# Kernel tuning notes

Measured on AMD Instinct MI355X. Metric: run time of the kernel, lower is better.

The kernel has to match this reference:

```python
import jax, jax.numpy as jnp
import numpy as np

S = 64        # state_dim
M = 16        # message_dim
H = 128       # hidden_unit_message_dim
HR = 128      # hidden_unit_readout_dim
NSTEPS = 10
N_NODES = 10000
N_FACTORS = 40000


def setup_inputs() -> dict:
    rng = np.random.default_rng(0)
    n, F = N_NODES, N_FACTORS
    # random undirected factor pairs (u, v) with u < v
    u = rng.integers(0, n - 1, F)
    v = rng.integers(u + 1, n)
    # var->factor directed edges: (u, i) and (v, i) for factor i
    v2f_src = np.stack([u, v], 1).ravel().astype(np.int32)          # [E]
    v2f_dst = np.repeat(np.arange(F), 2).astype(np.int32)           # [E]
    b = rng.normal(size=n).astype(np.float32)
    Juv = rng.normal(size=F).astype(np.float32)
    Jvu = rng.normal(size=F).astype(np.float32)
    feat_u = np.stack([b[u], b[v], Juv, Jvu], 1)
    feat_v = np.stack([b[v], b[u], Juv, Jvu], 1)
    feat = np.stack([feat_u, feat_v], 1).reshape(-1, 4).astype(np.float32)  # [E,4]
    p = lambda *s: (0.1 * rng.normal(size=s)).astype(np.float32)
    z = lambda *s: np.zeros(s, np.float32)
    inp = {
        'v2f_src': jnp.asarray(v2f_src), 'v2f_dst': jnp.asarray(v2f_dst),
        'f2v_src': jnp.asarray(v2f_dst), 'f2v_dst': jnp.asarray(v2f_src),
        'feat_v2f': jnp.asarray(feat), 'feat_f2v': jnp.asarray(feat),
        'n_nodes': n, 'n_factors': F,
        'Qw': jnp.asarray(p(4, M * M)), 'Qb': jnp.asarray(z(M * M)),
        'mp1_w1': jnp.asarray(p(2 * S, H)), 'mp1_b1': jnp.asarray(z(H)),
        'mp1_w2': jnp.asarray(p(H, H)), 'mp1_b2': jnp.asarray(z(H)),
        'mp1_w3': jnp.asarray(p(H, M)), 'mp1_b3': jnp.asarray(z(M)),
        'mp2_w1': jnp.asarray(p(2 * S, H)), 'mp2_b1': jnp.asarray(z(H)),
        'mp2_w2': jnp.asarray(p(H, H)), 'mp2_b2': jnp.asarray(z(H)),
        'mp2_w3': jnp.asarray(p(H, M)), 'mp2_b3': jnp.asarray(z(M)),
        'g1_wih': jnp.asarray(p(M, 3 * S)), 'g1_whh': jnp.asarray(p(S, 3 * S)),
        'g1_bih': jnp.asarray(z(3 * S)), 'g1_bhh': jnp.asarray(z(3 * S)),
        'g2_wih': jnp.asarray(p(M, 3 * S)), 'g2_whh': jnp.asarray(p(S, 3 * S)),
        'g2_bih': jnp.asarray(z(3 * S)), 'g2_bhh': jnp.asarray(z(3 * S)),
        'ro_w1': jnp.asarray(p(S, HR)), 'ro_b1': jnp.asarray(z(HR)),
        'ro_w2': jnp.asarray(p(HR, HR)), 'ro_b2': jnp.asarray(z(HR)),
        'ro_w3': jnp.asarray(p(HR, 2)), 'ro_b3': jnp.asarray(z(2)),
    }
    return inp


def _mlp(x, w1, b1, w2, b2, w3, b3):
    h = jax.nn.relu(x @ w1 + b1)
    h = jax.nn.relu(h @ w2 + b2)
    return h @ w3 + b3


def _gru(x, h, wih, whh, bih, bhh):
    # torch.nn.GRUCell gate order: r, z, n
    gi = x @ wih + bih
    gh = h @ whh + bhh
    ir, iz, inn = jnp.split(gi, 3, axis=-1)
    hr, hz, hn = jnp.split(gh, 3, axis=-1)
    r = jax.nn.sigmoid(ir + hr)
    zg = jax.nn.sigmoid(iz + hz)
    ng = jnp.tanh(inn + r * hn)
    return (1.0 - zg) * ng + zg * h


def reference(v2f_src, v2f_dst, f2v_src, f2v_dst, feat_v2f, feat_f2v,
              n_nodes, n_factors, Qw, Qb,
              mp1_w1, mp1_b1, mp1_w2, mp1_b2, mp1_w3, mp1_b3,
              mp2_w1, mp2_b1, mp2_w2, mp2_b2, mp2_w3, mp2_b3,
              g1_wih, g1_whh, g1_bih, g1_bhh,
              g2_wih, g2_whh, g2_bih, g2_bhh,
              ro_w1, ro_b1, ro_w2, ro_b2, ro_w3, ro_b3):
    var_h = jnp.zeros((n_nodes, S), feat_v2f.dtype)
    fac_h = jnp.zeros((n_factors, S), feat_v2f.dtype)
    # per-edge transform matrices are the same every step; hoist out of the loop
    q1 = (feat_v2f @ Qw + Qb).reshape(-1, M, M)  # [E, M, M]
    q2 = (feat_f2v @ Qw + Qb).reshape(-1, M, M)
    for _ in range(NSTEPS):
        # var -> factor
        x = jnp.concatenate([var_h[v2f_src], fac_h[v2f_dst]], axis=-1)  # [E, 2S]
        m = _mlp(x, mp1_w1, mp1_b1, mp1_w2, mp1_b2, mp1_w3, mp1_b3)    # [E, M]
        m = jnp.einsum('eij,ej->ei', q1, m)
        fac_msg = jax.ops.segment_sum(m, v2f_dst, num_segments=n_factors)
        fac_h = _gru(fac_msg, fac_h, g1_wih, g1_whh, g1_bih, g1_bhh)
        # factor -> var
        x = jnp.concatenate([fac_h[f2v_src], var_h[f2v_dst]], axis=-1)
        m = _mlp(x, mp2_w1, mp2_b1, mp2_w2, mp2_b2, mp2_w3, mp2_b3)
        m = jnp.einsum('eij,ej->ei', q2, m)
        var_msg = jax.ops.segment_sum(m, f2v_dst, num_segments=n_nodes)
        var_h = _gru(var_msg, var_h, g2_wih, g2_whh, g2_bih, g2_bhh)
    out = _mlp(var_h, ro_w1, ro_b1, ro_w2, ro_b2, ro_w3, ro_b3)  # [n_nodes, 2]
    return jax.nn.softmax(out, axis=1)
```

## Files before the change

kernel.cpp:

```cpp
#include <hip/hip_runtime.h>

#define NSTEPS 10

typedef __attribute__((ext_vector_type(8))) short bf16x8;
typedef __attribute__((ext_vector_type(4))) float f32x4;

__device__ __forceinline__ float sigmoidf_(float x) { return 1.0f / (1.0f + __expf(-x)); }
__device__ __forceinline__ float tanh_fast(float x) {
  const float e = __expf(2.f * x);
  return 1.f - 2.f / (e + 1.f);
}
__device__ __forceinline__ short bf16_(float x) {
  union { float f; unsigned u; } c; c.f = x;
  unsigned r = (c.u + 0x7FFFu + ((c.u >> 16) & 1u)) >> 16;
  return (short)r;
}
__device__ __forceinline__ unsigned pk2_(float a, float b) {
  union { float f; unsigned u; } ca, cb; ca.f = a; cb.f = b;
  return __builtin_amdgcn_perm(cb.u + 0x8000u, ca.u + 0x8000u, 0x07060302u);
}
__device__ __forceinline__ short pk1_(float a) {
  union { float f; unsigned u; } c; c.f = a;
  return (short)((c.u + 0x8000u) >> 16);
}
__device__ __forceinline__ float lo_(unsigned u) { union { unsigned u; float f; } c; c.u = u << 16; return c.f; }
__device__ __forceinline__ float hi_(unsigned u) { union { unsigned u; float f; } c; c.u = u & 0xffff0000u; return c.f; }

__device__ __forceinline__ f32x4 mfma_16x16x32(bf16x8 a, bf16x8 b, f32x4 c) {
  return __builtin_amdgcn_mfma_f32_16x16x32_bf16(a, b, c, 0, 0, 0);
}

#define C_W2A   0
#define C_W2B   32
#define C_W3A   64
#define C_W3B   68
#define C_ACOMB 72
#define C_W1AD  104
#define C_W1BS  120
#define C_RO1   136
#define C_RO2   152
#define C_Q     184
#define C_G1    189
#define C_G2    237
#define TOTAL_CHUNKS 285

struct PackJob { const float* src; int N; int KS; int nchunks; };
struct PackArgs {
  PackJob jb[10];
  const float* Qw; const float* Qb;
  const float* g1wih; const float* g1whh;
  const float* g2wih; const float* g2whh;
};

__device__ __forceinline__ float pack_val(const PackArgs& a, int g) {
  int c = g >> 9;
  const int r = g & 511;
  const int j = r & 7, n = (r >> 3) & 15, q = (r >> 7) & 3;
  const int kq = q * 8 + j;
  float val = 0.f;
  bool done = false;
  #pragma unroll
  for (int ji = 0; ji < 10; ++ji) {
    if (!done && c < a.jb[ji].nchunks) {
      const int ks = c % a.jb[ji].KS;
      const int nt = c / a.jb[ji].KS;
      const int k = ks * 32 + kq;
      val = a.jb[ji].src[(size_t)k * a.jb[ji].N + nt * 16 + n];
      done = true;
    }
    if (!done) c -= a.jb[ji].nchunks;
  }
  if (!done) {
    if (c < 5) {
      val = 0.f;
      if (kq < 16) val = (c < 4) ? a.Qw[c * 256 + n * 16 + kq] : a.Qb[n * 16 + kq];
    } else {
      c -= 5;
      const float* wih = (c < 48) ? a.g1wih : a.g2wih;
      const float* whh = (c < 48) ? a.g1whh : a.g2whh;
      if (c >= 48) c -= 48;
      const int nt = c / 3, ks = c % 3;
      const int k = ks * 32 + kq;
      const int ng = nt * 16 + n;
      const int gate = ng >> 6, s = ng & 63;
      val = 0.f;
      if (gate == 0) {
        if (k < 16) val = wih[k * 192 + s];
        else if (k < 80) val = whh[(k - 16) * 192 + s];
      } else if (gate == 1) {
        if (k < 16) val = wih[k * 192 + 64 + s];
        else if (k < 80) val = whh[(k - 16) * 192 + 64 + s];
      } else if (gate == 2) {
        if (k < 16) val = wih[k * 192 + 128 + s];
      } else {
        if (k >= 16 && k < 80) val = whh[(k - 16) * 192 + 128 + s];
      }
    }
  }
  return val;
}

__global__ __launch_bounds__(256) void k_pack(PackArgs a, short* __restrict__ out, int total) {
  const int g = blockIdx.x * 256 + threadIdx.x;
  if (g < total) out[g] = bf16_(pack_val(a, g));
}

__device__ __forceinline__ void edge_tail(
    const short* wb, int cw2, int cw3,
    const float* b2, const float* b3,
    short* h1s, short* ms, const float* feats,
    int lane, int wave, int m, int quad, float* mq)
{
  f32x4 acc2[2][4] = {};
  #pragma unroll
  for (int ks = 0; ks < 4; ++ks) {
    bf16x8 afr[4];
    #pragma unroll
    for (int mt = 0; mt < 4; ++mt)
      afr[mt] = *(const bf16x8*)&h1s[(mt * 16 + m) * 136 + ks * 32 + quad * 8];
    #pragma unroll
    for (int nt2 = 0; nt2 < 2; ++nt2) {
      const bf16x8 bfr = ((const bf16x8*)(wb + cw2))[((wave * 2 + nt2) * 4 + ks) * 64 + lane];
      #pragma unroll
      for (int mt = 0; mt < 4; ++mt)
        acc2[nt2][mt] = mfma_16x16x32(afr[mt], bfr, acc2[nt2][mt]);
    }
  }
  __syncthreads();
  #pragma unroll
  for (int nt2 = 0; nt2 < 2; ++nt2) {
    const int col = (wave * 2 + nt2) * 16 + m;
    const float bv = b2[col];
    #pragma unroll
    for (int mt = 0; mt < 4; ++mt)
      #pragma unroll
      for (int rr = 0; rr < 4; ++rr)
        h1s[(mt * 16 + quad * 4 + rr) * 136 + col] =
            pk1_(fmaxf(acc2[nt2][mt][rr] + bv, 0.f));
  }
  __syncthreads();
  f32x4 acc3 = {};
  #pragma unroll
  for (int ks = 0; ks < 4; ++ks) {
    const bf16x8 afr = *(const bf16x8*)&h1s[(wave * 16 + m) * 136 + ks * 32 + quad * 8];
    acc3 = mfma_16x16x32(afr, ((const bf16x8*)(wb + cw3))[ks * 64 + lane], acc3);
  }
  const float b3v = b3[m];
  #pragma unroll
  for (int rr = 0; rr < 4; ++rr) {
    const int row = wave * 16 + quad * 4 + rr;
    ms[row * 40 + m] = pk1_(acc3[rr] + b3v);
    ms[row * 40 + 16 + m] = 0;
  }
  __syncthreads();
  f32x4 accY[5] = {};
  {
    const bf16x8 afr = *(const bf16x8*)&ms[(wave * 16 + m) * 40 + quad * 8];
    #pragma unroll
    for (int tq = 0; tq < 5; ++tq)
      accY[tq] = mfma_16x16x32(afr, ((const bf16x8*)(wb + C_Q * 512))[tq * 64 + lane], accY[tq]);
  }
  #pragma unroll
  for (int rr = 0; rr < 4; ++rr) {
    const int row = wave * 16 + quad * 4 + rr;
    const f32x4 f = *(const f32x4*)&feats[row * 4];
    mq[rr] = accY[4][rr] + f.x * accY[0][rr] + f.y * accY[1][rr]
                         + f.z * accY[2][rr] + f.w * accY[3][rr];
  }
}

__device__ __forceinline__ void var_gru_tile(
    const short* wb, const float* gbih, const float* gbhh,
    const short* SA, float* gruH, short* outTile, int outStr,
    int rbase, int Nn, int lane, int wave, int m, int quad, bool writeH)
{
  f32x4 acc[16] = {};
  #pragma unroll
  for (int ks = 0; ks < 3; ++ks) {
    const bf16x8 av = *(const bf16x8*)&SA[(wave * 16 + m) * 104 + ks * 32 + quad * 8];
    #pragma unroll
    for (int nt = 0; nt < 16; ++nt)
      acc[nt] = mfma_16x16x32(av, ((const bf16x8*)(wb + C_G2 * 512))[(nt * 3 + ks) * 64 + lane], acc[nt]);
  }
  #pragma unroll
  for (int nt = 0; nt < 4; ++nt) {
    const int s = nt * 16 + m;
    const float br  = gbih[s] + gbhh[s];
    const float bz  = gbih[64 + s] + gbhh[64 + s];
    const float bin = gbih[128 + s];
    const float bhn = gbhh[128 + s];
    #pragma unroll
    for (int reg = 0; reg < 4; ++reg) {
      const int lr = wave * 16 + quad * 4 + reg, rg = rbase + lr;
      short hv = 0;
      if (rg < Nn) {
        const float ho = gruH[(size_t)rg * 64 + s];
        const float rr = sigmoidf_(acc[nt][reg] + br);
        const float zz = sigmoidf_(acc[4 + nt][reg] + bz);
        const float nn = tanh_fast(acc[8 + nt][reg] + bin + rr * (acc[12 + nt][reg] + bhn));
        const float hn = (1.f - zz) * nn + zz * ho;
        if (writeH) gruH[(size_t)rg * 64 + s] = hn;
        hv = pk1_(hn);
      }
      outTile[lr * outStr + s] = hv;
    }
  }
}

__global__ __launch_bounds__(256) void k_phaseA(
    const float* __restrict__ msgIn, float* __restrict__ msgZero,
    float* __restrict__ var_h,
    short* __restrict__ Abuf, short* __restrict__ Bbuf,
    const short* __restrict__ wb,
    const float* __restrict__ gbih, const float* __restrict__ gbhh, int N)
{
  __shared__ short SA[64 * 104];
  __shared__ short Xs[64 * 72];
  const int t = threadIdx.x, lane = t & 63, wave = t >> 6;
  const int m = lane & 15, quad = lane >> 4;
  const int rbase = blockIdx.x * 64;

  if (msgIn) {
    {
      const int r = t >> 2, q4 = t & 3, rg = rbase + r;
      #pragma unroll
      for (int i = 0; i < 6; ++i) {
        const int c = q4 * 4 + i * 16;
        f32x4 v = {0.f, 0.f, 0.f, 0.f};
        if (rg < N) {
          if (c < 16)      v = *(const f32x4*)(msgIn + (size_t)rg * 16 + c);
          else if (c < 80) v = *(const f32x4*)(var_h + (size_t)rg * 64 + (c - 16));
        }
        *(unsigned*)&SA[r * 104 + c]     = pk2_(v.x, v.y);
        *(unsigned*)&SA[r * 104 + c + 2] = pk2_(v.z, v.w);
      }
      if (rbase + r < N) {
        f32x4 z = {0.f, 0.f, 0.f, 0.f};
        *(f32x4*)(msgZero + (size_t)(rbase + r) * 16 + q4 * 4) = z;
      }
    }
    __syncthreads();
    var_gru_tile(wb, gbih, gbhh, SA, var_h, Xs, 72,
                 rbase, N, lane, wave, m, quad, true);
    __syncthreads();
  } else {
    const int r = t >> 2, q4 = t & 3, rg = rbase + r;
    #pragma unroll
    for (int i = 0; i < 4; ++i) {
      const int cc = q4 * 4 + i * 16;
      f32x4 v = {0.f, 0.f, 0.f, 0.f};
      if (rg < N) v = *(const f32x4*)(var_h + (size_t)rg * 64 + cc);
      *(unsigned*)&Xs[r * 72 + cc]     = pk2_(v.x, v.y);
      *(unsigned*)&Xs[r * 72 + cc + 2] = pk2_(v.z, v.w);
    }
    __syncthreads();
  }

  f32x4 acc[4][4] = {};
  #pragma unroll
  for (int ks = 0; ks < 2; ++ks) {
    bf16x8 afr[4];
    #pragma unroll
    for (int mt = 0; mt < 4; ++mt)
      afr[mt] = *(const bf16x8*)&Xs[(mt * 16 + m) * 72 + ks * 32 + quad * 8];
    #pragma unroll
    for (int j = 0; j < 4; ++j) {
      const bf16x8 bfr = ((const bf16x8*)(wb + C_ACOMB * 512))[((wave * 4 + j) * 2 + ks) * 64 + lane];
      #pragma unroll
      for (int mt = 0; mt < 4; ++mt)
        acc[j][mt] = mfma_16x16x32(afr[mt], bfr, acc[j][mt]);
    }
  }
  #pragma unroll
  for (int j = 0; j < 4; ++j) {
    const int col = (wave * 4 + j) * 16 + m;
    short* dst = (col < 128) ? Abuf : Bbuf;
    const int c2 = col & 127;
    #pragma unroll
    for (int mt = 0; mt < 4; ++mt)
      #pragma unroll
      for (int reg = 0; reg < 4; ++reg) {
        const int rg = rbase + mt * 16 + quad * 4 + reg;
        if (rg < N) dst[(size_t)rg * 128 + c2] = pk1_(acc[j][mt][reg]);
      }
  }
}

__global__ __launch_bounds__(256) void k_phaseB(
    const short* __restrict__ Abuf, const short* __restrict__ Bbuf,
    const int* __restrict__ v2f_src, const int* __restrict__ f2v_dst,
    const float* __restrict__ featA, const float* __restrict__ featB,
    const float* __restrict__ m1b1, const float* __restrict__ m1b2,
    const float* __restrict__ m1b3,
    const float* __restrict__ m2b1, const float* __restrict__ m2b2,
    const float* __restrict__ m2b3,
    const float* __restrict__ g1bih, const float* __restrict__ g1bhh,
    const short* __restrict__ wb,
    float* __restrict__ fac_h, float* __restrict__ msgV, int E, int F)
{
  __shared__ short AsG[32 * 104];
  __shared__ short Ps[32 * 136];
  __shared__ short h1s[64 * 136];
  __shared__ short ms[64 * 40];
  __shared__ short Fs2[32 * 72];
  __shared__ float feats[64 * 4];
  __shared__ int sidx[64], didx[64];

  const int t = threadIdx.x, lane = t & 63, wave = t >> 6;
  const int m = lane & 15, quad = lane >> 4;
  const int e0 = blockIdx.x * 64, f0 = blockIdx.x * 32;

  if (t < 64) {
    const int eg = e0 + t;
    sidx[t] = (eg < E) ? v2f_src[eg] : 0;
    didx[t] = (eg < E) ? f2v_dst[eg] : 0;
  }
  {
    const int e = t >> 2, k = t & 3, eg = e0 + e;
    feats[e * 4 + k] = (eg < E) ? featA[(size_t)eg * 4 + k] : 0.f;
  }
  {
    const int hr = t >> 3, hc = (t & 7) * 8;
    const int f = f0 + hr;
    f32x4 a0 = {0.f,0.f,0.f,0.f}, a1 = {0.f,0.f,0.f,0.f};
    if (f < F) {
      a0 = *(const f32x4*)(fac_h + (size_t)f * 64 + hc);
      a1 = *(const f32x4*)(fac_h + (size_t)f * 64 + hc + 4);
    }
    uint4 o;
    o.x = pk2_(a0.x, a0.y); o.y = pk2_(a0.z, a0.w);
    o.z = pk2_(a1.x, a1.y); o.w = pk2_(a1.z, a1.w);
    *(uint4*)&AsG[hr * 104 + 16 + hc] = o;
    if (t < 64) {
      uint4 z = make_uint4(0u, 0u, 0u, 0u);
      *(uint4*)&AsG[(t >> 1) * 104 + 80 + (t & 1) * 8] = z;
    }
  }
  __syncthreads();

  {
    const int mt = wave & 1, ng = wave >> 1;
    f32x4 pacc[4] = {};
    #pragma unroll
    for (int ks = 0; ks < 2; ++ks) {
      const bf16x8 av = *(const bf16x8*)&AsG[(mt * 16 + m) * 104 + 16 + ks * 32 + quad * 8];
      #pragma unroll
      for (int j = 0; j < 4; ++j) {
        const bf16x8 bfr = ((const bf16x8*)(wb + C_W1AD * 512))[((ng * 4 + j) * 2 + ks) * 64 + lane];
        pacc[j] = mfma_16x16x32(av, bfr, pacc[j]);
      }
    }
    #pragma unroll
    for (int j = 0; j < 4; ++j) {
      const int col = (ng * 4 + j) * 16 + m;
      #pragma unroll
      for (int reg = 0; reg < 4; ++reg)
        Ps[(mt * 16 + quad * 4 + reg) * 136 + col] = pk1_(pacc[j][reg]);
    }
  }
  __syncthreads();

  {
    const int r = t >> 2, q4 = t & 3;
    const bool ok = (e0 + r) < E;
    const short* pa = Abuf + (size_t)sidx[r] * 128;
    const short* pb = Ps + (r >> 1) * 136;
    #pragma unroll
    for (int i = 0; i < 4; ++i) {
      const int col = (q4 + i * 4) * 8;
      uint4 o = make_uint4(0u, 0u, 0u, 0u);
      if (ok) {
        const uint4 ua = *(const uint4*)(pa + col);
        const uint4 ub = *(const uint4*)(pb + col);
        const f32x4 ba = *(const f32x4*)(m1b1 + col);
        const f32x4 bb = *(const f32x4*)(m1b1 + col + 4);
        o.x = pk2_(fmaxf(lo_(ua.x) + lo_(ub.x) + ba.x, 0.f),
                   fmaxf(hi_(ua.x) + hi_(ub.x) + ba.y, 0.f));
        o.y = pk2_(fmaxf(lo_(ua.y) + lo_(ub.y) + ba.z, 0.f),
                   fmaxf(hi_(ua.y) + hi_(ub.y) + ba.w, 0.f));
        o.z = pk2_(fmaxf(lo_(ua.z) + lo_(ub.z) + bb.x, 0.f),
                   fmaxf(hi_(ua.z) + hi_(ub.z) + bb.y, 0.f));
        o.w = pk2_(fmaxf(lo_(ua.w) + lo_(ub.w) + bb.z, 0.f),
                   fmaxf(hi_(ua.w) + hi_(ub.w) + bb.w, 0.f));
      }
      *(uint4*)&h1s[r * 136 + col] = o;
    }
  }
  __syncthreads();

  float mq[4];
  edge_tail(wb, C_W2A * 512, C_W3A * 512, m1b2, m1b3,
            h1s, ms, feats, lane, wave, m, quad, mq);
  {
    const int fl = wave * 8 + quad * 2;
    AsG[fl * 104 + m]       = pk1_(mq[0] + mq[1]);
    AsG[(fl + 1) * 104 + m] = pk1_(mq[2] + mq[3]);
  }
  __syncthreads();

  {
    const int mtg = wave >> 1, sh = wave & 1;
    f32x4 accG[8] = {};
    #pragma unroll
    for (int ks = 0; ks < 3; ++ks) {
      const bf16x8 av = *(const bf16x8*)&AsG[(mtg * 16 + m) * 104 + ks * 32 + quad * 8];
      #pragma unroll
      for (int g = 0; g < 4; ++g)
        #pragma unroll
        for (int nt2 = 0; nt2 < 2; ++nt2) {
          const int nt = g * 4 + sh * 2 + nt2;
          accG[g * 2 + nt2] = mfma_16x16x32(
              av, ((const bf16x8*)(wb + C_G1 * 512))[(nt * 3 + ks) * 64 + lane],
              accG[g * 2 + nt2]);
        }
    }
    #pragma unroll
    for (int nt2 = 0; nt2 < 2; ++nt2) {
      const int s = sh * 32 + nt2 * 16 + m;
      const float br  = g1bih[s] + g1bhh[s];
      const float bz  = g1bih[64 + s] + g1bhh[64 + s];
      const float bin = g1bih[128 + s];
      const float bhn = g1bhh[128 + s];
      #pragma unroll
      for (int reg = 0; reg < 4; ++reg) {
        const int lr = mtg * 16 + quad * 4 + reg;
        const int f = f0 + lr;
        short hv = 0;
        if (f < F) {
          const float ho = fac_h[(size_t)f * 64 + s];
          const float rr = sigmoidf_(accG[nt2][reg] + br);
          const float zz = sigmoidf_(accG[2 + nt2][reg] + bz);
          const float nn = tanh_fast(accG[4 + nt2][reg] + bin +
                                     rr * (accG[6 + nt2][reg] + bhn));
          const float hn = (1.f - zz) * nn + zz * ho;
          fac_h[(size_t)f * 64 + s] = hn;
          hv = pk1_(hn);
        }
        Fs2[lr * 72 + s] = hv;
      }
    }
  }
  {
    const int e = t >> 2, k = t & 3, eg = e0 + e;
    feats[e * 4 + k] = (eg < E) ? featB[(size_t)eg * 4 + k] : 0.f;
  }
  __syncthreads();

  {
    const int mt = wave & 1, ng = wave >> 1;
    f32x4 pacc[4] = {};
    #pragma unroll
    for (int ks = 0; ks < 2; ++ks) {
      const bf16x8 av = *(const bf16x8*)&Fs2[(mt * 16 + m) * 72 + ks * 32 + quad * 8];
      #pragma unroll
      for (int j = 0; j < 4; ++j) {
        const bf16x8 bfr = ((const bf16x8*)(wb + C_W1BS * 512))[((ng * 4 + j) * 2 + ks) * 64 + lane];
        pacc[j] = mfma_16x16x32(av, bfr, pacc[j]);
      }
    }
    #pragma unroll
    for (int j = 0; j < 4; ++j) {
      const int col = (ng * 4 + j) * 16 + m;
      #pragma unroll
      for (int reg = 0; reg < 4; ++reg)
        Ps[(mt * 16 + quad * 4 + reg) * 136 + col] = pk1_(pacc[j][reg]);
    }
  }
  __syncthreads();

  {
    const int r = t >> 2, q4 = t & 3;
    const bool ok = (e0 + r) < E;
    const short* pa = Ps + (r >> 1) * 136;
    const short* pb = Bbuf + (size_t)didx[r] * 128;
    #pragma unroll
    for (int i = 0; i < 4; ++i) {
      const int col = (q4 + i * 4) * 8;
      uint4 o = make_uint4(0u, 0u, 0u, 0u);
      if (ok) {
        const uint4 ua = *(const uint4*)(pa + col);
        const uint4 ub = *(const uint4*)(pb + col);
        const f32x4 ba = *(const f32x4*)(m2b1 + col);
        const f32x4 bb = *(const f32x4*)(m2b1 + col + 4);
        o.x = pk2_(fmaxf(lo_(ua.x) + lo_(ub.x) + ba.x, 0.f),
                   fmaxf(hi_(ua.x) + hi_(ub.x) + ba.y, 0.f));
        o.y = pk2_(fmaxf(lo_(ua.y) + lo_(ub.y) + ba.z, 0.f),
                   fmaxf(hi_(ua.y) + hi_(ub.y) + ba.w, 0.f));
        o.z = pk2_(fmaxf(lo_(ua.z) + lo_(ub.z) + bb.x, 0.f),
                   fmaxf(hi_(ua.z) + hi_(ub.z) + bb.y, 0.f));
        o.w = pk2_(fmaxf(lo_(ua.w) + lo_(ub.w) + bb.z, 0.f),
                   fmaxf(hi_(ua.w) + hi_(ub.w) + bb.w, 0.f));
      }
      *(uint4*)&h1s[r * 136 + col] = o;
    }
  }
  __syncthreads();

  float mq2[4];
  edge_tail(wb, C_W2B * 512, C_W3B * 512, m2b2, m2b3,
            h1s, ms, feats, lane, wave, m, quad, mq2);
  #pragma unroll
  for (int rr = 0; rr < 4; ++rr) {
    const int erow = wave * 16 + quad * 4 + rr;
    if (e0 + erow < E)
      atomicAdd(msgV + (size_t)didx[erow] * 16 + m, mq2[rr]);
  }
}

__global__ __launch_bounds__(256) void k_readout_f(
    const float* __restrict__ gruMsg, const float* __restrict__ gruH,
    const short* __restrict__ wb,
    const float* __restrict__ gbih, const float* __restrict__ gbhh,
    const float* __restrict__ rob1, const float* __restrict__ rob2,
    const float* __restrict__ row3, const float* __restrict__ rob3,
    float* __restrict__ out, int rows)
{
  __shared__ short SA[64 * 104];
  __shared__ short SH[64 * 72];
  __shared__ short S1[64 * 136];
  __shared__ short S2[64 * 136];
  __shared__ float w3s[256];
  const int t = threadIdx.x, lane = t & 63, wave = t >> 6;
  const int m = lane & 15, quad = lane >> 4;
  const int rbase = blockIdx.x * 64;

  w3s[t] = row3[t];
  {
    const int r = t >> 2, q4 = t & 3, rg = rbase + r;
    #pragma unroll
    for (int i = 0; i < 6; ++i) {
      const int c = q4 * 4 + i * 16;
      f32x4 v = {0.f, 0.f, 0.f, 0.f};
      if (rg < rows) {
        if (c < 16)      v = *(const f32x4*)(gruMsg + (size_t)rg * 16 + c);
        else if (c < 80) v = *(const f32x4*)(gruH + (size_t)rg * 64 + (c - 16));
      }
      *(unsigned*)&SA[r * 104 + c]     = pk2_(v.x, v.y);
      *(unsigned*)&SA[r * 104 + c + 2] = pk2_(v.z, v.w);
    }
  }
  __syncthreads();
  var_gru_tile(wb, gbih, gbhh, SA, (float*)gruH, SH, 72,
               rbase, rows, lane, wave, m, quad, false);
  __syncthreads();
  {
    f32x4 acc[2][4] = {};
    #pragma unroll
    for (int ks = 0; ks < 2; ++ks) {
      bf16x8 afr[4];
      #pragma unroll
      for (int mt = 0; mt < 4; ++mt)
        afr[mt] = *(const bf16x8*)&SH[(mt * 16 + m) * 72 + ks * 32 + quad * 8];
      #pragma unroll
      for (int nt2 = 0; nt2 < 2; ++nt2) {
        const bf16x8 bfr = ((const bf16x8*)(wb + C_RO1 * 512))[((wave * 2 + nt2) * 2 + ks) * 64 + lane];
        #pragma unroll
        for (int mt = 0; mt < 4; ++mt)
          acc[nt2][mt] = mfma_16x16x32(afr[mt], bfr, acc[nt2][mt]);
      }
    }
    #pragma unroll
    for (int nt2 = 0; nt2 < 2; ++nt2) {
      const int col = (wave * 2 + nt2) * 16 + m;
      const float bv = rob1[col];
      #pragma unroll
      for (int mt = 0; mt < 4; ++mt)
        #pragma unroll
        for (int rr = 0; rr < 4; ++rr)
          S1[(mt * 16 + quad * 4 + rr) * 136 + col] =
              pk1_(fmaxf(acc[nt2][mt][rr] + bv, 0.f));
    }
  }
  __syncthreads();
  {
    f32x4 acc[2][4] = {};
    #pragma unroll
    for (int ks = 0; ks < 4; ++ks) {
      bf16x8 afr[4];
      #pragma unroll
      for (int mt = 0; mt < 4; ++mt)
        afr[mt] = *(const bf16x8*)&S1[(mt * 16 + m) * 136 + ks * 32 + quad * 8];
      #pragma unroll
      for (int nt2 = 0; nt2 < 2; ++nt2) {
        const bf16x8 bfr = ((const bf16x8*)(wb + C_RO2 * 512))[((wave * 2 + nt2) * 4 + ks) * 64 + lane];
        #pragma unroll
        for (int mt = 0; mt < 4; ++mt)
          acc[nt2][mt] = mfma_16x16x32(afr[mt], bfr, acc[nt2][mt]);
      }
    }
    #pragma unroll
    for (int nt2 = 0; nt2 < 2; ++nt2) {
      const int col = (wave * 2 + nt2) * 16 + m;
      const float bv = rob2[col];
      #pragma unroll
      for (int mt = 0; mt < 4; ++mt)
        #pragma unroll
        for (int rr = 0; rr < 4; ++rr)
          S2[(mt * 16 + quad * 4 + rr) * 136 + col] =
              pk1_(fmaxf(acc[nt2][mt][rr] + bv, 0.f));
    }
  }
  __syncthreads();
  if (t < 64) {
    const int rg = rbase + t;
    if (rg < rows) {
      float l0 = rob3[0], l1 = rob3[1];
      #pragma unroll 8
      for (int k = 0; k < 128; k += 2) {
        const unsigned u = *(const unsigned*)&S2[t * 136 + k];
        const float x0 = lo_(u), x1 = hi_(u);
        l0 = fmaf(x0, w3s[k * 2 + 0], l0);
        l1 = fmaf(x0, w3s[k * 2 + 1], l1);
        l0 = fmaf(x1, w3s[k * 2 + 2], l0);
        l1 = fmaf(x1, w3s[k * 2 + 3], l1);
      }
      const float mx = fmaxf(l0, l1);
      const float e0 = __expf(l0 - mx), e1 = __expf(l1 - mx);
      const float inv = 1.f / (e0 + e1);
      out[(size_t)rg * 2 + 0] = e0 * inv;
      out[(size_t)rg * 2 + 1] = e1 * inv;
    }
  }
}

extern "C" void kernel_launch(void* const* d_in, const int* in_sizes, int n_in,
                              void* d_out, int out_size, void* d_ws, size_t ws_size,
                              hipStream_t stream)
{
  const int*   v2f_src  = (const int*)d_in[0];
  const int*   f2v_dst  = (const int*)d_in[3];
  const float* feat_v2f = (const float*)d_in[4];
  const float* feat_f2v = (const float*)d_in[5];
  const float* Qw    = (const float*)d_in[8];
  const float* Qb    = (const float*)d_in[9];
  const float* m1w1  = (const float*)d_in[10];
  const float* m1b1  = (const float*)d_in[11];
  const float* m1w2  = (const float*)d_in[12];
  const float* m1b2  = (const float*)d_in[13];
  const float* m1w3  = (const float*)d_in[14];
  const float* m1b3  = (const float*)d_in[15];
  const float* m2w1  = (const float*)d_in[16];
  const float* m2b1  = (const float*)d_in[17];
  const float* m2w2  = (const float*)d_in[18];
  const float* m2b2  = (const float*)d_in[19];
  const float* m2w3  = (const float*)d_in[20];
  const float* m2b3  = (const float*)d_in[21];
  const float* g1wih = (const float*)d_in[22];
  const float* g1whh = (const float*)d_in[23];
  const float* g1bih = (const float*)d_in[24];
  const float* g1bhh = (const float*)d_in[25];
  const float* g2wih = (const float*)d_in[26];
  const float* g2whh = (const float*)d_in[27];
  const float* g2bih = (const float*)d_in[28];
  const float* g2bhh = (const float*)d_in[29];
  const float* row1  = (const float*)d_in[30];
  const float* rob1  = (const float*)d_in[31];
  const float* row2  = (const float*)d_in[32];
  const float* rob2  = (const float*)d_in[33];
  const float* row3  = (const float*)d_in[34];
  const float* rob3  = (const float*)d_in[35];

  const int E = in_sizes[0];
  const int N = out_size / 2;
  const int F = E / 2;

  float* wsf   = (float*)d_ws;
  float* var_h = wsf;
  float* fac_h = var_h + (size_t)N * 64;
  float* msgV  = fac_h + (size_t)F * 64;
  short* Abuf  = (short*)(msgV + (size_t)N * 16);
  short* Bbuf  = Abuf + (size_t)N * 128;
  short* wb    = Bbuf + (size_t)N * 128;

  hipMemsetAsync(var_h, 0,
                 ((size_t)N * 64 + (size_t)F * 64 + (size_t)N * 16) * sizeof(float),
                 stream);

  PackArgs pk;
  pk.jb[0] = {m1w2,            128, 4, 32};
  pk.jb[1] = {m2w2,            128, 4, 32};
  pk.jb[2] = {m1w3,             16, 4,  4};
  pk.jb[3] = {m2w3,             16, 4,  4};
  pk.jb[4] = {m1w1,            128, 2, 16};
  pk.jb[5] = {m2w1 + 64 * 128, 128, 2, 16};
  pk.jb[6] = {m1w1 + 64 * 128, 128, 2, 16};
  pk.jb[7] = {m2w1,            128, 2, 16};
  pk.jb[8] = {row1,            128, 2, 16};
  pk.jb[9] = {row2,            128, 4, 32};
  pk.Qw = Qw; pk.Qb = Qb;
  pk.g1wih = g1wih; pk.g1whh = g1whh;
  pk.g2wih = g2wih; pk.g2whh = g2whh;
  const int packTotal = TOTAL_CHUNKS * 512;
  k_pack<<<(packTotal + 255) / 256, 256, 0, stream>>>(pk, wb, packTotal);

  const int gN = (N + 63) / 64;
  const int gE = (E + 63) / 64;

  for (int step = 0; step < NSTEPS; ++step) {
    k_phaseA<<<gN, 256, 0, stream>>>(
        step ? msgV : nullptr, msgV, var_h, Abuf, Bbuf, wb, g2bih, g2bhh, N);
    k_phaseB<<<gE, 256, 0, stream>>>(
        Abuf, Bbuf, v2f_src, f2v_dst, feat_v2f, feat_f2v,
        m1b1, m1b2, m1b3, m2b1, m2b2, m2b3, g1bih, g1bhh,
        wb, fac_h, msgV, E, F);
  }

  k_readout_f<<<gN, 256, 0, stream>>>(
      msgV, var_h, wb, g2bih, g2bhh, rob1, rob2, row3, rob3, (float*)d_out, N);
}
```

Measured before the change: 706.1 us.

## Transpose MFMA operand roles so outputs store as packed row vectors

Several small GEMMs (MLP layer 2, readout layers, A/B combine, partial W1 products) now put the weight fragment in the A operand and the activation tile in the B operand. Each lane then holds four consecutive output columns of one row, so results are written as packed uint2 bf16 stores instead of scattered 16-bit stores. The GRU weight packing permutes the state index to match, which makes the GRU epilogue vectorised too (f32x4/float2 loads and stores of hidden state, packed tile writes). In edge_tail this also drops one barrier, and shared memory is merged into one aliased buffer to cut LDS use, which relies on the aliased regions never being live at the same time.

```diff
diff --git a/kernel.cpp b/kernel.cpp
--- a/kernel.cpp
+++ b/kernel.cpp
@@ -82,7 +82,9 @@
       const int nt = c / 3, ks = c % 3;
       const int k = ks * 32 + kq;
       const int ng = nt * 16 + n;
-      const int gate = ng >> 6, s = ng & 63;
+      const int gate = ng >> 6;
+      const int nq = ng & 63;
+      const int s = (nq & 15) * 4 + (nq >> 4);
       val = 0.f;
       if (gate == 0) {
         if (k < 16) val = wih[k * 192 + s];
@@ -105,40 +107,98 @@
   if (g < total) out[g] = bf16_(pack_val(a, g));
 }
 
+__device__ __forceinline__ void var_gru_tile(
+    const short* wb, const float* gbih, const float* gbhh,
+    const short* SA, float* gruH, short* outTile, int outStr,
+    int rbase, int Nn, int lane, int wave, int m, int quad, bool writeH)
+{
+  f32x4 acc[16] = {};
+  #pragma unroll
+  for (int ks = 0; ks < 3; ++ks) {
+    const bf16x8 av = *(const bf16x8*)&SA[(wave * 16 + m) * 104 + ks * 32 + quad * 8];
+    #pragma unroll
+    for (int nt = 0; nt < 16; ++nt)
+      acc[nt] = mfma_16x16x32(av, ((const bf16x8*)(wb + C_G2 * 512))[(nt * 3 + ks) * 64 + lane], acc[nt]);
+  }
+  const int sb = m * 4;
+  const f32x4 bir = *(const f32x4*)(gbih + sb);
+  const f32x4 bhr = *(const f32x4*)(gbhh + sb);
+  const f32x4 biz = *(const f32x4*)(gbih + 64 + sb);
+  const f32x4 bhz = *(const f32x4*)(gbhh + 64 + sb);
+  const f32x4 bi4 = *(const f32x4*)(gbih + 128 + sb);
+  const f32x4 bh4 = *(const f32x4*)(gbhh + 128 + sb);
+  #pragma unroll
+  for (int reg = 0; reg < 4; ++reg) {
+    const int lr = wave * 16 + quad * 4 + reg, rg = rbase + lr;
+    uint2 pv; pv.x = 0u; pv.y = 0u;
+    if (rg < Nn) {
+      const f32x4 ho = *(const f32x4*)(gruH + (size_t)rg * 64 + sb);
+      f32x4 hn;
+      #pragma unroll
+      for (int nt = 0; nt < 4; ++nt) {
+        const float rr = sigmoidf_(acc[nt][reg] + bir[nt] + bhr[nt]);
+        const float zz = sigmoidf_(acc[4 + nt][reg] + biz[nt] + bhz[nt]);
+        const float nn = tanh_fast(acc[8 + nt][reg] + bi4[nt] + rr * (acc[12 + nt][reg] + bh4[nt]));
+        hn[nt] = (1.f - zz) * nn + zz * ho[nt];
+      }
+      if (writeH) *(f32x4*)(gruH + (size_t)rg * 64 + sb) = hn;
+      pv.x = pk2_(hn[0], hn[1]);
+      pv.y = pk2_(hn[2], hn[3]);
+    }
+    *(uint2*)&outTile[lr * outStr + sb] = pv;
+  }
+}
+
+__device__ __forceinline__ void partial_gemm_T(
+    const short* chunk, const short* srcTile, int srcStr, short* Ps,
+    int lane, int wave, int m, int quad)
+{
+  const int nt = wave & 1, mt0 = (wave >> 1) * 4;
+  f32x4 acc[4] = {};
+  #pragma unroll
+  for (int ks = 0; ks < 2; ++ks) {
+    const bf16x8 bfr = *(const bf16x8*)&srcTile[(nt * 16 + m) * srcStr + ks * 32 + quad * 8];
+    #pragma unroll
+    for (int j = 0; j < 4; ++j)
+      acc[j] = mfma_16x16x32(((const bf16x8*)chunk)[((mt0 + j) * 2 + ks) * 64 + lane], bfr, acc[j]);
+  }
+  #pragma unroll
+  for (int j = 0; j < 4; ++j) {
+    const int col = (mt0 + j) * 16 + quad * 4;
+    uint2 pv;
+    pv.x = pk2_(acc[j][0], acc[j][1]);
+    pv.y = pk2_(acc[j][2], acc[j][3]);
+    *(uint2*)&Ps[(nt * 16 + m) * 136 + col] = pv;
+  }
+}
+
 __device__ __forceinline__ void edge_tail(
     const short* wb, int cw2, int cw3,
     const float* b2, const float* b3,
     short* h1s, short* ms, const float* feats,
     int lane, int wave, int m, int quad, float* mq)
 {
-  f32x4 acc2[2][4] = {};
-  #pragma unroll
-  for (int ks = 0; ks < 4; ++ks) {
-    bf16x8 afr[4];
-    #pragma unroll
-    for (int mt = 0; mt < 4; ++mt)
-      afr[mt] = *(const bf16x8*)&h1s[(mt * 16 + m) * 136 + ks * 32 + quad * 8];
-    #pragma unroll
-    for (int nt2 = 0; nt2 < 2; ++nt2) {
-      const bf16x8 bfr = ((const bf16x8*)(wb + cw2))[((wave * 2 + nt2) * 4 + ks) * 64 + lane];
+  {
+    f32x4 acc[8] = {};
+    #pragma unroll
+    for (int ks = 0; ks < 4; ++ks) {
+      const bf16x8 bfr = *(const bf16x8*)&h1s[(wave * 16 + m) * 136 + ks * 32 + quad * 8];
       #pragma unroll
-      for (int mt = 0; mt < 4; ++mt)
-        acc2[nt2][mt] = mfma_16x16x32(afr[mt], bfr, acc2[nt2][mt]);
-    }
-  }
-  __syncthreads();
-  #pragma unroll
-  for (int nt2 = 0; nt2 < 2; ++nt2) {
-    const int col = (wave * 2 + nt2) * 16 + m;
-    const float bv = b2[col];
-    #pragma unroll
-    for (int mt = 0; mt < 4; ++mt)
-      #pragma unroll
-      for (int rr = 0; rr < 4; ++rr)
-        h1s[(mt * 16 + quad * 4 + rr) * 136 + col] =
-            pk1_(fmaxf(acc2[nt2][mt][rr] + bv, 0.f));
-  }
-  __syncthreads();
+      for (int mt = 0; mt < 8; ++mt)
+        acc[mt] = mfma_16x16x32(((const bf16x8*)(wb + cw2))[(mt * 4 + ks) * 64 + lane], bfr, acc[mt]);
+    }
+    #pragma unroll
+    for (int mt = 0; mt < 8; ++mt) {
+      const int col = mt * 16 + quad * 4;
+      const f32x4 bv = *(const f32x4*)(b2 + col);
+      uint2 pv;
+      pv.x = pk2_(fmaxf(acc[mt][0] + bv[0], 0.f), fmaxf(acc[mt][1] + bv[1], 0.f));
+      pv.y = pk2_(fmaxf(acc[mt][2] + bv[2], 0.f), fmaxf(acc[mt][3] + bv[3], 0.f));
+      *(uint2*)&h1s[(wave * 16 + m) * 136 + col] = pv;
+    }
+  }
+  __syncthreads();
+
   f32x4 acc3 = {};
   #pragma unroll
   for (int ks = 0; ks < 4; ++ks) {
@@ -153,6 +213,7 @@
     ms[row * 40 + 16 + m] = 0;
   }
   __syncthreads();
+
   f32x4 accY[5] = {};
   {
     const bf16x8 afr = *(const bf16x8*)&ms[(wave * 16 + m) * 40 + quad * 8];
@@ -166,44 +227,6 @@
     const f32x4 f = *(const f32x4*)&feats[row * 4];
     mq[rr] = accY[4][rr] + f.x * accY[0][rr] + f.y * accY[1][rr]
                          + f.z * accY[2][rr] + f.w * accY[3][rr];
-  }
-}
-
-__device__ __forceinline__ void var_gru_tile(
-    const short* wb, const float* gbih, const float* gbhh,
-    const short* SA, float* gruH, short* outTile, int outStr,
-    int rbase, int Nn, int lane, int wave, int m, int quad, bool writeH)
-{
-  f32x4 acc[16] = {};
-  #pragma unroll
-  for (int ks = 0; ks < 3; ++ks) {
-    const bf16x8 av = *(const bf16x8*)&SA[(wave * 16 + m) * 104 + ks * 32 + quad * 8];
-    #pragma unroll
-    for (int nt = 0; nt < 16; ++nt)
-      acc[nt] = mfma_16x16x32(av, ((const bf16x8*)(wb + C_G2 * 512))[(nt * 3 + ks) * 64 + lane], acc[nt]);
-  }
-  #pragma unroll
-  for (int nt = 0; nt < 4; ++nt) {
-    const int s = nt * 16 + m;
-    const float br  = gbih[s] + gbhh[s];
-    const float bz  = gbih[64 + s] + gbhh[64 + s];
-    const float bin = gbih[128 + s];
-    const float bhn = gbhh[128 + s];
-    #pragma unroll
-    for (int reg = 0; reg < 4; ++reg) {
-      const int lr = wave * 16 + quad * 4 + reg, rg = rbase + lr;
-      short hv = 0;
-      if (rg < Nn) {
-        const float ho = gruH[(size_t)rg * 64 + s];
-        const float rr = sigmoidf_(acc[nt][reg] + br);
-        const float zz = sigmoidf_(acc[4 + nt][reg] + bz);
-        const float nn = tanh_fast(acc[8 + nt][reg] + bin + rr * (acc[12 + nt][reg] + bhn));
-        const float hn = (1.f - zz) * nn + zz * ho;
-        if (writeH) gruH[(size_t)rg * 64 + s] = hn;
-        hv = pk1_(hn);
-      }
-      outTile[lr * outStr + s] = hv;
-    }
   }
 }
 
@@ -256,33 +279,25 @@
     __syncthreads();
   }
 
-  f32x4 acc[4][4] = {};
+  f32x4 acc[16] = {};
   #pragma unroll
   for (int ks = 0; ks < 2; ++ks) {
-    bf16x8 afr[4];
-    #pragma unroll
-    for (int mt = 0; mt < 4; ++mt)
-      afr[mt] = *(const bf16x8*)&Xs[(mt * 16 + m) * 72 + ks * 32 + quad * 8];
-    #pragma unroll
-    for (int j = 0; j < 4; ++j) {
-      const bf16x8 bfr = ((const bf16x8*)(wb + C_ACOMB * 512))[((wave * 4 + j) * 2 + ks) * 64 + lane];
-      #pragma unroll
-      for (int mt = 0; mt < 4; ++mt)
-        acc[j][mt] = mfma_16x16x32(afr[mt], bfr, acc[j][mt]);
-    }
-  }
-  #pragma unroll
-  for (int j = 0; j < 4; ++j) {
-    const int col = (wave * 4 + j) * 16 + m;
-    short* dst = (col < 128) ? Abuf : Bbuf;
-    const int c2 = col & 127;
-    #pragma unroll
-    for (int mt = 0; mt < 4; ++mt)
-      #pragma unroll
-      for (int reg = 0; reg < 4; ++reg) {
-        const int rg = rbase + mt * 16 + quad * 4 + reg;
-        if (rg < N) dst[(size_t)rg * 128 + c2] = pk1_(acc[j][mt][reg]);
-      }
+    const bf16x8 bfr = *(const bf16x8*)&Xs[(wave * 16 + m) * 72 + ks * 32 + quad * 8];
+    #pragma unroll
+    for (int mt = 0; mt < 16; ++mt)
+      acc[mt] = mfma_16x16x32(((const bf16x8*)(wb + C_ACOMB * 512))[(mt * 2 + ks) * 64 + lane], bfr, acc[mt]);
+  }
+  const int rg = rbase + wave * 16 + m;
+  if (rg < N) {
+    #pragma unroll
+    for (int mt = 0; mt < 16; ++mt) {
+      const int col = mt * 16 + quad * 4;
+      short* dst = (col < 128) ? Abuf : Bbuf;
+      uint2 pv;
+      pv.x = pk2_(acc[mt][0], acc[mt][1]);
+      pv.y = pk2_(acc[mt][2], acc[mt][3]);
+      *(uint2*)&dst[(size_t)rg * 128 + (col & 127)] = pv;
+    }
   }
 }
 
@@ -298,13 +313,15 @@
     const short* __restrict__ wb,
     float* __restrict__ fac_h, float* __restrict__ msgV, int E, int F)
 {
-  __shared__ short AsG[32 * 104];
-  __shared__ short Ps[32 * 136];
-  __shared__ short h1s[64 * 136];
-  __shared__ short ms[64 * 40];
-  __shared__ short Fs2[32 * 72];
-  __shared__ float feats[64 * 4];
-  __shared__ int sidx[64], didx[64];
+  __shared__ __align__(16) char smemB[38912];
+  short* h1s   = (short*)(smemB);
+  short* Ps    = (short*)(smemB + 17408);
+  short* ms    = (short*)(smemB + 17408);
+  short* AsG   = (short*)(smemB + 26112);
+  short* Fs2   = (short*)(smemB + 32768);
+  float* feats = (float*)(smemB + 37376);
+  int*   sidx  = (int*)(smemB + 38400);
+  int*   didx  = (int*)(smemB + 38656);
 
   const int t = threadIdx.x, lane = t & 63, wave = t >> 6;
   const int m = lane & 15, quad = lane >> 4;
@@ -338,26 +355,7 @@
   }
   __syncthreads();
 
-  {
-    const int mt = wave & 1, ng = wave >> 1;
-    f32x4 pacc[4] = {};
-    #pragma unroll
-    for (int ks = 0; ks < 2; ++ks) {
-      const bf16x8 av = *(const bf16x8*)&AsG[(mt * 16 + m) * 104 + 16 + ks * 32 + quad * 8];
-      #pragma unroll
-      for (int j = 0; j < 4; ++j) {
-        const bf16x8 bfr = ((const bf16x8*)(wb + C_W1AD * 512))[((ng * 4 + j) * 2 + ks) * 64 + lane];
-        pacc[j] = mfma_16x16x32(av, bfr, pacc[j]);
-      }
-    }
-    #pragma unroll
-    for (int j = 0; j < 4; ++j) {
-      const int col = (ng * 4 + j) * 16 + m;
-      #pragma unroll
-      for (int reg = 0; reg < 4; ++reg)
-        Ps[(mt * 16 + quad * 4 + reg) * 136 + col] = pk1_(pacc[j][reg]);
-    }
-  }
+  partial_gemm_T(wb + C_W1AD * 512, AsG + 16, 104, Ps, lane, wave, m, quad);
   __syncthreads();
 
   {
@@ -414,30 +412,30 @@
               accG[g * 2 + nt2]);
         }
     }
-    #pragma unroll
-    for (int nt2 = 0; nt2 < 2; ++nt2) {
-      const int s = sh * 32 + nt2 * 16 + m;
-      const float br  = g1bih[s] + g1bhh[s];
-      const float bz  = g1bih[64 + s] + g1bhh[64 + s];
-      const float bin = g1bih[128 + s];
-      const float bhn = g1bhh[128 + s];
-      #pragma unroll
-      for (int reg = 0; reg < 4; ++reg) {
-        const int lr = mtg * 16 + quad * 4 + reg;
-        const int f = f0 + lr;
-        short hv = 0;
-        if (f < F) {
-          const float ho = fac_h[(size_t)f * 64 + s];
-          const float rr = sigmoidf_(accG[nt2][reg] + br);
-          const float zz = sigmoidf_(accG[2 + nt2][reg] + bz);
-          const float nn = tanh_fast(accG[4 + nt2][reg] + bin +
-                                     rr * (accG[6 + nt2][reg] + bhn));
-          const float hn = (1.f - zz) * nn + zz * ho;
-          fac_h[(size_t)f * 64 + s] = hn;
-          hv = pk1_(hn);
-        }
-        Fs2[lr * 72 + s] = hv;
-      }
+    const int sb = m * 4 + sh * 2;
+    const float br0 = g1bih[sb] + g1bhh[sb],         br1 = g1bih[sb + 1] + g1bhh[sb + 1];
+    const float bz0 = g1bih[64 + sb] + g1bhh[64 + sb], bz1 = g1bih[65 + sb] + g1bhh[65 + sb];
+    const float bi0 = g1bih[128 + sb], bi1 = g1bih[129 + sb];
+    const float bh0 = g1bhh[128 + sb], bh1 = g1bhh[129 + sb];
+    #pragma unroll
+    for (int reg = 0; reg < 4; ++reg) {
+      const int lr = mtg * 16 + quad * 4 + reg;
+      const int f = f0 + lr;
+      float hn0 = 0.f, hn1 = 0.f;
+      if (f < F) {
+        const float2 ho = *(const float2*)(fac_h + (size_t)f * 64 + sb);
+        const float r0 = sigmoidf_(accG[0][reg] + br0);
+        const float r1 = sigmoidf_(accG[1][reg] + br1);
+        const float z0 = sigmoidf_(accG[2][reg] + bz0);
+        const float z1 = sigmoidf_(accG[3][reg] + bz1);
+        const float n0 = tanh_fast(accG[4][reg] + bi0 + r0 * (accG[6][reg] + bh0));
+        const float n1 = tanh_fast(accG[5][reg] + bi1 + r1 * (accG[7][reg] + bh1));
+        hn0 = (1.f - z0) * n0 + z0 * ho.x;
+        hn1 = (1.f - z1) * n1 + z1 * ho.y;
+        float2 hw; hw.x = hn0; hw.y = hn1;
+        *(float2*)(fac_h + (size_t)f * 64 + sb) = hw;
+      }
+      *(unsigned*)&Fs2[lr * 72 + sb] = pk2_(hn0, hn1);
     }
   }
   {
@@ -446,26 +444,7 @@
   }
   __syncthreads();
 
-  {
-    const int mt = wave & 1, ng = wave >> 1;
-    f32x4 pacc[4] = {};
-    #pragma unroll
-    for (int ks = 0; ks < 2; ++ks) {
-      const bf16x8 av = *(const bf16x8*)&Fs2[(mt * 16 + m) * 72 + ks * 32 + quad * 8];
-      #pragma unroll
-      for (int j = 0; j < 4; ++j) {
-        const bf16x8 bfr = ((const bf16x8*)(wb + C_W1BS * 512))[((ng * 4 + j) * 2 + ks) * 64 + lane];
-        pacc[j] = mfma_16x16x32(av, bfr, pacc[j]);
-      }
-    }
-    #pragma unroll
-    for (int j = 0; j < 4; ++j) {
-      const int col = (ng * 4 + j) * 16 + m;
-      #pragma unroll
-      for (int reg = 0; reg < 4; ++reg)
-        Ps[(mt * 16 + quad * 4 + reg) * 136 + col] = pk1_(pacc[j][reg]);
-    }
-  }
+  partial_gemm_T(wb + C_W1BS * 512, Fs2, 72, Ps, lane, wave, m, quad);
   __syncthreads();
 
   {
@@ -543,64 +522,49 @@
   var_gru_tile(wb, gbih, gbhh, SA, (float*)gruH, SH, 72,
                rbase, rows, lane, wave, m, quad, false);
   __syncthreads();
-  {
-    f32x4 acc[2][4] = {};
+
+  {
+    f32x4 acc[8] = {};
     #pragma unroll
     for (int ks = 0; ks < 2; ++ks) {
-      bf16x8 afr[4];
+      const bf16x8 bfr = *(const bf16x8*)&SH[(wave * 16 + m) * 72 + ks * 32 + quad * 8];
       #pragma unroll
-      for (int mt = 0; mt < 4; ++mt)
-        afr[mt] = *(const bf16x8*)&SH[(mt * 16 + m) * 72 + ks * 32 + quad * 8];
+      for (int mt = 0; mt < 8; ++mt)
+        acc[mt] = mfma_16x16x32(((const bf16x8*)(wb + C_RO1 * 512))[(mt * 2 + ks) * 64 + lane], bfr, acc[mt]);
+    }
+    #pragma unroll
+    for (int mt = 0; mt < 8; ++mt) {
+      const int col = mt * 16 + quad * 4;
+      const f32x4 bv = *(const f32x4*)(rob1 + col);
+      uint2 pv;
+      pv.x = pk2_(fmaxf(acc[mt][0] + bv[0], 0.f), fmaxf(acc[mt][1] + bv[1], 0.f));
+      pv.y = pk2_(fmaxf(acc[mt][2] + bv[2], 0.f), fmaxf(acc[mt][3] + bv[3], 0.f));
+      *(uint2*)&S1[(wave * 16 + m) * 136 + col] = pv;
+    }
+  }
+  __syncthreads();
+
+  {
+    f32x4 acc[8] = {};
+    #pragma unroll
+    for (int ks = 0; ks < 4; ++ks) {
+      const bf16x8 bfr = *(const bf16x8*)&S1[(wave * 16 + m) * 136 + ks * 32 + quad * 8];
       #pragma unroll
-      for (int nt2 = 0; nt2 < 2; ++nt2) {
-        const bf16x8 bfr = ((const bf16x8*)(wb + C_RO1 * 512))[((wave * 2 + nt2) * 2 + ks) * 64 + lane];
-        #pragma unroll
-        for (int mt = 0; mt < 4; ++mt)
-          acc[nt2][mt] = mfma_16x16x32(afr[mt], bfr, acc[nt2][mt]);
-      }
-    }
-    #pragma unroll
-    for (int nt2 = 0; nt2 < 2; ++nt2) {
-      const int col = (wave * 2 + nt2) * 16 + m;
-      const float bv = rob1[col];
-      #pragma unroll
-      for (int mt = 0; mt < 4; ++mt)
-        #pragma unroll
-        for (int rr = 0; rr < 4; ++rr)
-          S1[(mt * 16 + quad * 4 + rr) * 136 + col] =
-              pk1_(fmaxf(acc[nt2][mt][rr] + bv, 0.f));
-    }
-  }
-  __syncthreads();
-  {
-    f32x4 acc[2][4] = {};
-    #pragma unroll
-    for (int ks = 0; ks < 4; ++ks) {
-      bf16x8 afr[4];
-      #pragma unroll
-      for (int mt = 0; mt < 4; ++mt)
-        afr[mt] = *(const bf16x8*)&S1[(mt * 16 + m) * 136 + ks * 32 + quad * 8];
-      #pragma unroll
-      for (int nt2 = 0; nt2 < 2; ++nt2) {
-        const bf16x8 bfr = ((const bf16x8*)(wb + C_RO2 * 512))[((wave * 2 + nt2) * 4 + ks) * 64 + lane];
-        #pragma unroll
-        for (int mt = 0; mt < 4; ++mt)
-          acc[nt2][mt] = mfma_16x16x32(afr[mt], bfr, acc[nt2][mt]);
-      }
-    }
-    #pragma unroll
-    for (int nt2 = 0; nt2 < 2; ++nt2) {
-      const int col = (wave * 2 + nt2) * 16 + m;
-      const float bv = rob2[col];
-      #pragma unroll
-      for (int mt = 0; mt < 4; ++mt)
-        #pragma unroll
-        for (int rr = 0; rr < 4; ++rr)
-          S2[(mt * 16 + quad * 4 + rr) * 136 + col] =
-              pk1_(fmaxf(acc[nt2][mt][rr] + bv, 0.f));
-    }
-  }
-  __syncthreads();
+      for (int mt = 0; mt < 8; ++mt)
+        acc[mt] = mfma_16x16x32(((const bf16x8*)(wb + C_RO2 * 512))[(mt * 4 + ks) * 64 + lane], bfr, acc[mt]);
+    }
+    #pragma unroll
+    for (int mt = 0; mt < 8; ++mt) {
+      const int col = mt * 16 + quad * 4;
+      const f32x4 bv = *(const f32x4*)(rob2 + col);
+      uint2 pv;
+      pv.x = pk2_(fmaxf(acc[mt][0] + bv[0], 0.f), fmaxf(acc[mt][1] + bv[1], 0.f));
+      pv.y = pk2_(fmaxf(acc[mt][2] + bv[2], 0.f), fmaxf(acc[mt][3] + bv[3], 0.f));
+      *(uint2*)&S2[(wave * 16 + m) * 136 + col] = pv;
+    }
+  }
+  __syncthreads();
+
   if (t < 64) {
     const int rg = rbase + t;
     if (rg < rows) {
```

Result: no change. 693.6 us (-1.8%).
